# Optimization experiments

Measured on AMD Instinct MI355X. Metric: run time of the kernel, lower is better.

## Reference

```python
import jax, jax.numpy as jnp
import numpy as np

N, E, D, H, L = 20000, 320000, 128, 8, 3
C = D // H  # per-head channels = 16


def setup_inputs() -> dict:
    key = jax.random.key(0)
    ks = jax.random.split(key, 20)
    s = 1.0 / np.sqrt(D)
    inp = {
        "x": jax.random.normal(ks[0], (N, D), dtype=jnp.float32),
        "edge_index": jax.random.randint(ks[1], (2, E), 0, N, dtype=jnp.int64),
        "Wq": jax.random.normal(ks[2], (L, D, D), dtype=jnp.float32) * s,
        "bq": jnp.zeros((L, D), dtype=jnp.float32),
        "Wk": jax.random.normal(ks[3], (L, D, D), dtype=jnp.float32) * s,
        "bk": jnp.zeros((L, D), dtype=jnp.float32),
        "Wv": jax.random.normal(ks[4], (L, D, D), dtype=jnp.float32) * s,
        "bv": jnp.zeros((L, D), dtype=jnp.float32),
        "Wskip": jax.random.normal(ks[5], (L, D, D), dtype=jnp.float32) * s,
        "bskip": jnp.zeros((L, D), dtype=jnp.float32),
        "Wbeta": jax.random.normal(ks[6], (L, 3 * D, 1), dtype=jnp.float32) * (1.0 / np.sqrt(3 * D)),
        "ln_g": jnp.ones((L, D), dtype=jnp.float32),
        "ln_b": jnp.zeros((L, D), dtype=jnp.float32),
        "Wout": jax.random.normal(ks[7], (D, D), dtype=jnp.float32) * s,
        "bout": jnp.zeros((D,), dtype=jnp.float32),
    }
    return inp


def _layer_norm(x, g, b, eps=1e-5):
    mu = jnp.mean(x, axis=-1, keepdims=True)
    var = jnp.mean(jnp.square(x - mu), axis=-1, keepdims=True)
    return (x - mu) * jax.lax.rsqrt(var + eps) * g + b


def _transformer_conv(x, src, dst, Wq, bq, Wk, bk, Wv, bv, Wskip, bskip, Wbeta):
    # project q/k/v: [N, D] -> [N, H, C]
    q = (x @ Wq + bq).reshape(N, H, C)
    k = (x @ Wk + bk).reshape(N, H, C)
    v = (x @ Wv + bv).reshape(N, H, C)
    # per-edge attention logits: [E, H]
    alpha = jnp.sum(q[dst] * k[src], axis=-1) / np.sqrt(C)
    # scatter-softmax over edges grouped by dst node
    m = jax.ops.segment_max(alpha, dst, num_segments=N)  # [N, H]
    m = jnp.where(jnp.isfinite(m), m, 0.0)
    ea = jnp.exp(alpha - m[dst])
    denom = jax.ops.segment_sum(ea, dst, num_segments=N)  # [N, H]
    attn = ea / (denom[dst] + 1e-16)  # [E, H]
    # weighted message aggregation: [N, H, C] -> [N, D]
    out = jax.ops.segment_sum(attn[:, :, None] * v[src], dst, num_segments=N)
    out = out.reshape(N, D)
    # beta-gated skip connection (beta=True, root_weight=True)
    x_r = x @ Wskip + bskip
    beta = jax.nn.sigmoid(jnp.concatenate([out, x_r, out - x_r], axis=-1) @ Wbeta)  # [N, 1]
    return beta * x_r + (1.0 - beta) * out


def reference(x, edge_index, Wq, bq, Wk, bk, Wv, bv, Wskip, bskip, Wbeta, ln_g, ln_b, Wout, bout):
    src, dst = edge_index[0], edge_index[1]
    for i in range(L):
        residual = x
        x = _transformer_conv(x, src, dst, Wq[i], bq[i], Wk[i], bk[i], Wv[i], bv[i],
                              Wskip[i], bskip[i], Wbeta[i])
        x = jax.nn.relu(x)  # dropout is identity in eval mode
        x = _layer_norm(x + residual, ln_g[i], ln_b[i])
    return x @ Wout + bout
```

## Files before the change

kernel.cpp:

```cpp
#include <hip/hip_runtime.h>

#define N_NODES 20000
#define N_EDGES 320000
#define DIM 128
#define NLAYER 3
#define SCAN_BLK 1024
#define N_SCAN_BLKS ((N_NODES + SCAN_BLK - 1) / SCAN_BLK)
#define LDS_STRIDE 136

#define PREP_CASTX_BLKS 2500
#define PREP_CASTW_BLKS 208
#define PREP_ZERO_BLKS 79
#define PREP_TOTAL (PREP_CASTX_BLKS + PREP_CASTW_BLKS + PREP_ZERO_BLKS)

typedef __attribute__((ext_vector_type(8))) short short8;
typedef __attribute__((ext_vector_type(4))) float f32x4;

__device__ inline ushort f2bf(float f) {
  uint u = __float_as_uint(f);
  uint r = (u + 0x7fffu + ((u >> 16) & 1u)) >> 16;
  return (ushort)r;
}
__device__ inline float bf2f(ushort u) { return __uint_as_float(((uint)u) << 16); }

__global__ __launch_bounds__(256) void prep_kernel(
    const float* __restrict__ x, ushort* __restrict__ xb,
    const float* __restrict__ Wq, const float* __restrict__ Wk,
    const float* __restrict__ Wv, const float* __restrict__ Ws,
    const float* __restrict__ Wo, ushort* __restrict__ wt,
    int* __restrict__ degc) {
  int b = blockIdx.x;
  int t = threadIdx.x;
  if (b < PREP_CASTX_BLKS) {
    int i = b * 256 + t;
    float4 f = ((const float4*)x)[i];
    ushort4 o;
    o.x = f2bf(f.x); o.y = f2bf(f.y); o.z = f2bf(f.z); o.w = f2bf(f.w);
    ((ushort4*)xb)[i] = o;
  } else if (b < PREP_CASTX_BLKS + PREP_CASTW_BLKS) {
    int idx = b - PREP_CASTX_BLKS;
    int z = idx >> 4;
    int r = idx & 15;
    int k0 = (r >> 2) * 32, n0 = (r & 3) * 32;
    const float* src;
    if (z < 12) {
      int l = z >> 2, j = z & 3;
      src = (j == 0 ? Wq : j == 1 ? Wk : j == 2 ? Wv : Ws) + (size_t)l * DIM * DIM;
    } else {
      src = Wo;
    }
    __shared__ float tile[32][33];
    int tx = t & 31, ty = t >> 5;
    #pragma unroll
    for (int i = 0; i < 32; i += 8)
      tile[ty + i][tx] = src[(size_t)(k0 + ty + i) * DIM + n0 + tx];
    __syncthreads();
    ushort* dst = wt + (size_t)z * DIM * DIM;
    #pragma unroll
    for (int i = 0; i < 32; i += 8)
      dst[(size_t)(n0 + ty + i) * DIM + k0 + tx] = f2bf(tile[tx][ty + i]);
  } else {
    int i = (b - PREP_CASTX_BLKS - PREP_CASTW_BLKS) * 256 + t;
    if (i < N_NODES) degc[i] = 0;
  }
}


__global__ void count_deg_kernel(const int* __restrict__ ei, int* __restrict__ deg) {
  int e = blockIdx.x * 256 + threadIdx.x;
  if (e < N_EDGES) atomicAdd(&deg[ei[N_EDGES + e]], 1);
}

__global__ __launch_bounds__(SCAN_BLK) void scan1_kernel(const int* __restrict__ deg,
                                                         int* __restrict__ rowptr,
                                                         int* __restrict__ blksum) {
  __shared__ int wsum[16];
  int t = threadIdx.x, lane = t & 63, w = t >> 6;
  int i = blockIdx.x * SCAN_BLK + t;
  int val = (i < N_NODES) ? deg[i] : 0;
  int s = val;
  #pragma unroll
  for (int off = 1; off < 64; off <<= 1) {
    int u = __shfl_up(s, off);
    if (lane >= off) s += u;
  }
  if (lane == 63) wsum[w] = s;
  __syncthreads();
  if (t < 16) {
    int wv = wsum[t];
    int ss = wv;
    #pragma unroll
    for (int off = 1; off < 16; off <<= 1) {
      int u = __shfl_up(ss, off);
      if (t >= off) ss += u;
    }
    wsum[t] = ss - wv;
  }
  __syncthreads();
  int excl = wsum[w] + s - val;
  if (i < N_NODES) rowptr[i] = excl;
  if (t == SCAN_BLK - 1) blksum[blockIdx.x] = excl + val;
}

__global__ void scan2_kernel(int* __restrict__ blksum, int* __restrict__ rowptr) {
  int t = threadIdx.x;
  int val = (t < N_SCAN_BLKS) ? blksum[t] : 0;
  int s = val;
  #pragma unroll
  for (int off = 1; off < 64; off <<= 1) {
    int u = __shfl_up(s, off);
    if (t >= off) s += u;
  }
  if (t < N_SCAN_BLKS) blksum[t] = s - val;
  if (t == 63) rowptr[N_NODES] = s;
}

__global__ __launch_bounds__(SCAN_BLK) void scan3_kernel(int* __restrict__ rowptr,
                                                         const int* __restrict__ blksum,
                                                         int* __restrict__ degc) {
  int i = blockIdx.x * SCAN_BLK + threadIdx.x;
  if (i < N_NODES) {
    rowptr[i] += blksum[blockIdx.x];
    degc[i] = 0;
  }
}

__global__ void scatter_kernel(const int* __restrict__ ei, const int* __restrict__ rowptr,
                               int* __restrict__ cursor, int* __restrict__ csr_src) {
  int e = blockIdx.x * 256 + threadIdx.x;
  if (e < N_EDGES) {
    int d = ei[N_EDGES + e];
    int s = ei[e];
    int pos = atomicAdd(&cursor[d], 1);
    csr_src[rowptr[d] + pos] = s;
  }
}

template <int OUT_BF16>
__global__ __launch_bounds__(256) void gemm_mfma_kernel(
    const ushort* __restrict__ X, const ushort* __restrict__ WT,
    const float* __restrict__ B0, const float* __restrict__ B1,
    const float* __restrict__ B2, const float* __restrict__ B3,
    void* __restrict__ O0, void* __restrict__ O1, void* __restrict__ O2,
    void* __restrict__ O3, int st0, int st1, int st2, int st3) {
  __shared__ ushort As[128 * LDS_STRIDE];
  int mat = blockIdx.y;
  const ushort* Wt = WT + (size_t)mat * DIM * DIM;
  const float* bias;
  void* O;
  int ost;
  switch (mat) {
    case 0: bias = B0; O = O0; ost = st0; break;
    case 1: bias = B1; O = O1; ost = st1; break;
    case 2: bias = B2; O = O2; ost = st2; break;
    default: bias = B3; O = O3; ost = st3; break;
  }
  int t = threadIdx.x;
  int wid = t >> 6, lane = t & 63;
  int row0 = blockIdx.x * 128;
  int wr = wid >> 1, wc = wid & 1;
  int lr = lane & 15;
  int kc8 = (lane >> 4) * 8;

  {
    int rowi = t >> 4;
    int col = (t & 15) * 8;
    #pragma unroll
    for (int pass = 0; pass < 8; ++pass) {
      int row = pass * 16 + rowi;
      int gr = min(row0 + row, N_NODES - 1);
      short8 val = *(const short8*)(X + (size_t)gr * DIM + col);
      *(short8*)(As + row * LDS_STRIDE + col) = val;
    }
  }
  __syncthreads();

  f32x4 acc[4][4];
  #pragma unroll
  for (int i = 0; i < 4; ++i)
    #pragma unroll
    for (int j = 0; j < 4; ++j) acc[i][j] = (f32x4){0.f, 0.f, 0.f, 0.f};

  #pragma unroll
  for (int ks = 0; ks < 4; ++ks) {
    short8 b[4];
    #pragma unroll
    for (int cf = 0; cf < 4; ++cf) {
      int c = wc * 64 + cf * 16 + lr;
      b[cf] = *(const short8*)(Wt + (size_t)c * DIM + ks * 32 + kc8);
    }
    #pragma unroll
    for (int rf = 0; rf < 4; ++rf) {
      int r = wr * 64 + rf * 16 + lr;
      short8 a = *(const short8*)(As + r * LDS_STRIDE + ks * 32 + kc8);
      #pragma unroll
      for (int cf = 0; cf < 4; ++cf)
        acc[rf][cf] = __builtin_amdgcn_mfma_f32_16x16x32_bf16(a, b[cf], acc[rf][cf], 0, 0, 0);
    }
  }

  #pragma unroll
  for (int cf = 0; cf < 4; ++cf) {
    int c = wc * 64 + cf * 16 + lr;
    float bv = bias[c];
    #pragma unroll
    for (int rf = 0; rf < 4; ++rf) {
      #pragma unroll
      for (int reg = 0; reg < 4; ++reg) {
        int r = row0 + wr * 64 + rf * 16 + (lane >> 4) * 4 + reg;
        if (r < N_NODES) {
          float val = acc[rf][cf][reg] + bv;
          if (OUT_BF16)
            ((ushort*)O)[(size_t)r * ost + c] = f2bf(val);
          else
            ((float*)O)[(size_t)r * ost + c] = val;
        }
      }
    }
  }
}

__global__ __launch_bounds__(256) void attn_fused_kernel(
    const ushort* __restrict__ q, const ushort* __restrict__ kv,
    const ushort* __restrict__ xr, const float* __restrict__ xres,
    const int* __restrict__ rowptr, const int* __restrict__ csr_src,
    const float* __restrict__ wbeta, const float* __restrict__ lng,
    const float* __restrict__ lnb, float* __restrict__ xnext,
    ushort* __restrict__ xnextb) {
  __shared__ float lds_s[4][8][20];
  int w = threadIdx.x >> 6;
  int lane = threadIdx.x & 63;
  int n = blockIdx.x * 4 + w;
  int h = lane & 7, e = lane >> 3;

  const ushort* qrow = q + (size_t)n * DIM + h * 16;
  short8 q0 = *(const short8*)qrow;
  short8 q1 = *(const short8*)(qrow + 8);
  float qf[16];
  #pragma unroll
  for (int i = 0; i < 8; ++i) {
    qf[i] = bf2f((ushort)q0[i]);
    qf[8 + i] = bf2f((ushort)q1[i]);
  }

  int s0 = rowptr[n];
  int deg = rowptr[n + 1] - s0;
  float acc[16];
  #pragma unroll
  for (int i = 0; i < 16; ++i) acc[i] = 0.f;
  float dsum = 0.f;

  for (int base = 0; base < deg; base += 8) {
    int idx = base + e;
    bool valid = idx < deg;
    int src = csr_src[s0 + min(idx, deg - 1)];
    const ushort* kr = kv + (size_t)src * 256 + h * 16;
    short8 ka = *(const short8*)kr;
    short8 kb2 = *(const short8*)(kr + 8);
    short8 va = *(const short8*)(kr + 128);
    short8 vb2 = *(const short8*)(kr + 136);
    float p0 = 0.f, p1 = 0.f;
    #pragma unroll
    for (int i = 0; i < 8; ++i) {
      p0 = fmaf(qf[i], bf2f((ushort)ka[i]), p0);
      p1 = fmaf(qf[8 + i], bf2f((ushort)kb2[i]), p1);
    }
    float ea = __expf((p0 + p1) * 0.25f);
    ea = valid ? ea : 0.f;
    dsum += ea;
    #pragma unroll
    for (int i = 0; i < 8; ++i) {
      acc[i] = fmaf(ea, bf2f((ushort)va[i]), acc[i]);
      acc[8 + i] = fmaf(ea, bf2f((ushort)vb2[i]), acc[8 + i]);
    }
  }

  #pragma unroll
  for (int off = 8; off <= 32; off <<= 1) {
    dsum += __shfl_xor(dsum, off);
    #pragma unroll
    for (int i = 0; i < 16; ++i) acc[i] += __shfl_xor(acc[i], off);
  }
  if (lane < 8) {
    #pragma unroll
    for (int i = 0; i < 16; i += 4)
      *(float4*)&lds_s[w][lane][i] = make_float4(acc[i], acc[i + 1], acc[i + 2], acc[i + 3]);
    lds_s[w][lane][16] = dsum;
  }
  __syncthreads();

  int c0 = lane * 2;
  int hh = lane >> 3, cc = (lane & 7) * 2;
  float2 ov = *(float2*)&lds_s[w][hh][cc];
  float den = lds_s[w][hh][16];
  float inv = 1.f / (den + 1e-16f);
  float o0 = ov.x * inv, o1 = ov.y * inv;

  ushort2 xru = *(const ushort2*)(xr + (size_t)n * DIM + c0);
  float xr0 = bf2f(xru.x), xr1 = bf2f(xru.y);
  float wa0 = wbeta[c0] + wbeta[2 * DIM + c0];
  float wa1 = wbeta[c0 + 1] + wbeta[2 * DIM + c0 + 1];
  float wb0 = wbeta[DIM + c0] - wbeta[2 * DIM + c0];
  float wb1 = wbeta[DIM + c0 + 1] - wbeta[2 * DIM + c0 + 1];
  float bs = o0 * wa0 + o1 * wa1 + xr0 * wb0 + xr1 * wb1;
  #pragma unroll
  for (int off = 1; off < 64; off <<= 1) bs += __shfl_xor(bs, off);
  float beta = 1.f / (1.f + __expf(-bs));
  float y0 = fmaxf(beta * xr0 + (1.f - beta) * o0, 0.f);
  float y1 = fmaxf(beta * xr1 + (1.f - beta) * o1, 0.f);
  float2 rv = *(const float2*)(xres + (size_t)n * DIM + c0);
  y0 += rv.x;
  y1 += rv.y;
  float s = y0 + y1;
  #pragma unroll
  for (int off = 1; off < 64; off <<= 1) s += __shfl_xor(s, off);
  float mu = s * (1.f / 128.f);
  float d0 = y0 - mu, d1 = y1 - mu;
  float vs = d0 * d0 + d1 * d1;
  #pragma unroll
  for (int off = 1; off < 64; off <<= 1) vs += __shfl_xor(vs, off);
  float rstd = rsqrtf(vs * (1.f / 128.f) + 1e-5f);
  float2 g = *(const float2*)(lng + c0);
  float2 b = *(const float2*)(lnb + c0);
  float out0 = d0 * rstd * g.x + b.x;
  float out1 = d1 * rstd * g.y + b.y;
  *(float2*)(xnext + (size_t)n * DIM + c0) = make_float2(out0, out1);
  ushort2 ob;
  ob.x = f2bf(out0);
  ob.y = f2bf(out1);
  *(ushort2*)(xnextb + (size_t)n * DIM + c0) = ob;
}


extern "C" void kernel_launch(void* const* d_in, const int* in_sizes, int n_in,
                              void* d_out, int out_size, void* d_ws, size_t ws_size,
                              hipStream_t stream) {
  const float* x_in = (const float*)d_in[0];
  const int* ei = (const int*)d_in[1];
  const float* Wq = (const float*)d_in[2];
  const float* bq = (const float*)d_in[3];
  const float* Wk = (const float*)d_in[4];
  const float* bk = (const float*)d_in[5];
  const float* Wv = (const float*)d_in[6];
  const float* bv = (const float*)d_in[7];
  const float* Wsk = (const float*)d_in[8];
  const float* bsk = (const float*)d_in[9];
  const float* Wb = (const float*)d_in[10];
  const float* lng = (const float*)d_in[11];
  const float* lnb = (const float*)d_in[12];
  const float* Wout = (const float*)d_in[13];
  const float* bout = (const float*)d_in[14];
  float* out = (float*)d_out;

  char* p = (char*)d_ws;
  auto alloc = [&](size_t bytes) {
    char* r = p;
    p += (bytes + 255) & ~(size_t)255;
    return r;
  };
  const size_t NB2 = (size_t)N_NODES * DIM * 2;
  const size_t NB4 = (size_t)N_NODES * DIM * 4;
  ushort* xbb = (ushort*)alloc(NB2);
  ushort* qb = (ushort*)alloc(NB2);
  ushort* kvb = (ushort*)alloc(NB2 * 2);
  ushort* xrb = (ushort*)alloc(NB2);
  float* xf0 = (float*)alloc(NB4);
  float* xf1 = (float*)alloc(NB4);
  ushort* wt = (ushort*)alloc((size_t)13 * DIM * DIM * 2);
  int* rowptr = (int*)alloc((N_NODES + 1) * 4);
  int* degc = (int*)alloc(N_NODES * 4);
  int* blksum = (int*)alloc(64 * 4);
  int* csr_src = (int*)alloc(N_EDGES * 4);

  prep_kernel<<<PREP_TOTAL, 256, 0, stream>>>(x_in, xbb, Wq, Wk, Wv, Wsk, Wout, wt, degc);

  count_deg_kernel<<<(N_EDGES + 255) / 256, 256, 0, stream>>>(ei, degc);
  scan1_kernel<<<N_SCAN_BLKS, SCAN_BLK, 0, stream>>>(degc, rowptr, blksum);
  scan2_kernel<<<1, 64, 0, stream>>>(blksum, rowptr);
  scan3_kernel<<<N_SCAN_BLKS, SCAN_BLK, 0, stream>>>(rowptr, blksum, degc);
  scatter_kernel<<<(N_EDGES + 255) / 256, 256, 0, stream>>>(ei, rowptr, degc, csr_src);

  const int GX = (N_NODES + 127) / 128;
  const float* xres = x_in;
  float* xfbufs[NLAYER] = {xf0, xf1, xf0};
  for (int l = 0; l < NLAYER; ++l) {
    gemm_mfma_kernel<1><<<dim3(GX, 4), 256, 0, stream>>>(
        xbb, wt + (size_t)l * 4 * DIM * DIM,
        bq + (size_t)l * DIM, bk + (size_t)l * DIM, bv + (size_t)l * DIM,
        bsk + (size_t)l * DIM,
        qb, kvb, kvb + 128, xrb, DIM, 256, 256, DIM);
    attn_fused_kernel<<<N_NODES / 4, 256, 0, stream>>>(
        qb, kvb, xrb, xres, rowptr, csr_src,
        Wb + (size_t)l * 3 * DIM, lng + (size_t)l * DIM, lnb + (size_t)l * DIM,
        xfbufs[l], xbb);
    xres = xfbufs[l];
  }
  gemm_mfma_kernel<0><<<dim3(GX, 1), 256, 0, stream>>>(
      xbb, wt + (size_t)12 * DIM * DIM, bout, bout, bout, bout,
      out, out, out, out, DIM, DIM, DIM, DIM);
}
```

Measured before the change: 217.7 us.

## Store K/V head-major and split attention into per-head gather and epilogue kernels

The QKV GEMM now writes K and V into a head-major layout where each node's 16 K and 16 V values for one head sit together in a 64-byte record. Attention is split into a gather kernel with one block per (head, 4 nodes), where 4 lanes share one edge and 16 edges are processed per step, and a separate epilogue kernel for the beta gate, residual and layer norm. The aim is to make the per-head K/V table small and contiguous, so random gathers hit cache better and the grid has more parallelism. In exchange, the attention output makes an extra fp32 round trip through memory, there is one more launch per layer, and the scattered per-element GEMM stores may coalesce less well.

```diff
diff --git a/kernel.cpp b/kernel.cpp
--- a/kernel.cpp
+++ b/kernel.cpp
@@ -142,18 +142,18 @@
     const float* __restrict__ B0, const float* __restrict__ B1,
     const float* __restrict__ B2, const float* __restrict__ B3,
     void* __restrict__ O0, void* __restrict__ O1, void* __restrict__ O2,
-    void* __restrict__ O3, int st0, int st1, int st2, int st3) {
+    void* __restrict__ O3, int m0, int m1, int m2, int m3) {
   __shared__ ushort As[128 * LDS_STRIDE];
   int mat = blockIdx.y;
   const ushort* Wt = WT + (size_t)mat * DIM * DIM;
   const float* bias;
   void* O;
-  int ost;
+  int mode;
   switch (mat) {
-    case 0: bias = B0; O = O0; ost = st0; break;
-    case 1: bias = B1; O = O1; ost = st1; break;
-    case 2: bias = B2; O = O2; ost = st2; break;
-    default: bias = B3; O = O3; ost = st3; break;
+    case 0: bias = B0; O = O0; mode = m0; break;
+    case 1: bias = B1; O = O1; mode = m1; break;
+    case 2: bias = B2; O = O2; mode = m2; break;
+    default: bias = B3; O = O3; mode = m3; break;
   }
   int t = threadIdx.x;
   int wid = t >> 6, lane = t & 63;
@@ -210,91 +210,79 @@
         int r = row0 + wr * 64 + rf * 16 + (lane >> 4) * 4 + reg;
         if (r < N_NODES) {
           float val = acc[rf][cf][reg] + bv;
-          if (OUT_BF16)
-            ((ushort*)O)[(size_t)r * ost + c] = f2bf(val);
-          else
-            ((float*)O)[(size_t)r * ost + c] = val;
+          if (OUT_BF16) {
+            ushort v16 = f2bf(val);
+            if (mode == 0)
+              ((ushort*)O)[(size_t)r * DIM + c] = v16;
+            else
+              ((ushort*)O)[(size_t)(c >> 4) * (N_NODES * 32) + (size_t)r * 32 +
+                           (c & 15) + (mode == 2 ? 16 : 0)] = v16;
+          } else {
+            ((float*)O)[(size_t)r * DIM + c] = val;
+          }
         }
       }
     }
   }
 }
 
-__global__ __launch_bounds__(256) void attn_fused_kernel(
-    const ushort* __restrict__ q, const ushort* __restrict__ kv,
-    const ushort* __restrict__ xr, const float* __restrict__ xres,
+__global__ __launch_bounds__(256) void attn_gather_kernel(
+    const ushort* __restrict__ q, const ushort* __restrict__ kvh,
     const int* __restrict__ rowptr, const int* __restrict__ csr_src,
-    const float* __restrict__ wbeta, const float* __restrict__ lng,
-    const float* __restrict__ lnb, float* __restrict__ xnext,
-    ushort* __restrict__ xnextb) {
-  __shared__ float lds_s[4][8][20];
-  int w = threadIdx.x >> 6;
-  int lane = threadIdx.x & 63;
-  int n = blockIdx.x * 4 + w;
-  int h = lane & 7, e = lane >> 3;
-
-  const ushort* qrow = q + (size_t)n * DIM + h * 16;
-  short8 q0 = *(const short8*)qrow;
-  short8 q1 = *(const short8*)(qrow + 8);
-  float qf[16];
-  #pragma unroll
-  for (int i = 0; i < 8; ++i) {
-    qf[i] = bf2f((ushort)q0[i]);
-    qf[8 + i] = bf2f((ushort)q1[i]);
-  }
-
+    float* __restrict__ aout) {
+  int w = threadIdx.x >> 6, lane = threadIdx.x & 63;
+  int h = blockIdx.x & 7;
+  int n = (blockIdx.x >> 3) * 4 + w;
+  int e = lane >> 2, qq = lane & 3;
+  ushort4 qu = *(const ushort4*)(q + (size_t)n * DIM + h * 16 + qq * 4);
+  float qf0 = bf2f(qu.x), qf1 = bf2f(qu.y), qf2 = bf2f(qu.z), qf3 = bf2f(qu.w);
   int s0 = rowptr[n];
   int deg = rowptr[n + 1] - s0;
-  float acc[16];
-  #pragma unroll
-  for (int i = 0; i < 16; ++i) acc[i] = 0.f;
-  float dsum = 0.f;
-
-  for (int base = 0; base < deg; base += 8) {
-    int idx = base + e;
+  const ushort* bh = kvh + (size_t)h * (N_NODES * 32);
+  float dsum = 0.f, va0 = 0.f, va1 = 0.f, va2 = 0.f, va3 = 0.f;
+  for (int b0 = 0; b0 < deg; b0 += 16) {
+    int idx = b0 + e;
     bool valid = idx < deg;
     int src = csr_src[s0 + min(idx, deg - 1)];
-    const ushort* kr = kv + (size_t)src * 256 + h * 16;
-    short8 ka = *(const short8*)kr;
-    short8 kb2 = *(const short8*)(kr + 8);
-    short8 va = *(const short8*)(kr + 128);
-    short8 vb2 = *(const short8*)(kr + 136);
-    float p0 = 0.f, p1 = 0.f;
-    #pragma unroll
-    for (int i = 0; i < 8; ++i) {
-      p0 = fmaf(qf[i], bf2f((ushort)ka[i]), p0);
-      p1 = fmaf(qf[8 + i], bf2f((ushort)kb2[i]), p1);
-    }
-    float ea = __expf((p0 + p1) * 0.25f);
+    const ushort* rec = bh + (size_t)src * 32 + qq * 4;
+    ushort4 ku = *(const ushort4*)rec;
+    ushort4 vu = *(const ushort4*)(rec + 16);
+    float part = qf0 * bf2f(ku.x) + qf1 * bf2f(ku.y) + qf2 * bf2f(ku.z) + qf3 * bf2f(ku.w);
+    part += __shfl_xor(part, 1);
+    part += __shfl_xor(part, 2);
+    float ea = __expf(part * 0.25f);
     ea = valid ? ea : 0.f;
     dsum += ea;
-    #pragma unroll
-    for (int i = 0; i < 8; ++i) {
-      acc[i] = fmaf(ea, bf2f((ushort)va[i]), acc[i]);
-      acc[8 + i] = fmaf(ea, bf2f((ushort)vb2[i]), acc[8 + i]);
-    }
-  }
-
-  #pragma unroll
-  for (int off = 8; off <= 32; off <<= 1) {
+    va0 = fmaf(ea, bf2f(vu.x), va0);
+    va1 = fmaf(ea, bf2f(vu.y), va1);
+    va2 = fmaf(ea, bf2f(vu.z), va2);
+    va3 = fmaf(ea, bf2f(vu.w), va3);
+  }
+  #pragma unroll
+  for (int off = 4; off <= 32; off <<= 1) {
     dsum += __shfl_xor(dsum, off);
-    #pragma unroll
-    for (int i = 0; i < 16; ++i) acc[i] += __shfl_xor(acc[i], off);
-  }
-  if (lane < 8) {
-    #pragma unroll
-    for (int i = 0; i < 16; i += 4)
-      *(float4*)&lds_s[w][lane][i] = make_float4(acc[i], acc[i + 1], acc[i + 2], acc[i + 3]);
-    lds_s[w][lane][16] = dsum;
-  }
-  __syncthreads();
-
+    va0 += __shfl_xor(va0, off);
+    va1 += __shfl_xor(va1, off);
+    va2 += __shfl_xor(va2, off);
+    va3 += __shfl_xor(va3, off);
+  }
+  if (e == 0) {
+    float inv = 1.f / (dsum + 1e-16f);
+    float4 o = make_float4(va0 * inv, va1 * inv, va2 * inv, va3 * inv);
+    *(float4*)(aout + (size_t)n * DIM + h * 16 + qq * 4) = o;
+  }
+}
+
+__global__ __launch_bounds__(256) void attn_epi_kernel(
+    const float* __restrict__ aout, const ushort* __restrict__ xr,
+    const float* __restrict__ xres, const float* __restrict__ wbeta,
+    const float* __restrict__ lng, const float* __restrict__ lnb,
+    float* __restrict__ xnext, ushort* __restrict__ xnextb) {
+  int w = threadIdx.x >> 6, lane = threadIdx.x & 63;
+  int n = blockIdx.x * 4 + w;
   int c0 = lane * 2;
-  int hh = lane >> 3, cc = (lane & 7) * 2;
-  float2 ov = *(float2*)&lds_s[w][hh][cc];
-  float den = lds_s[w][hh][16];
-  float inv = 1.f / (den + 1e-16f);
-  float o0 = ov.x * inv, o1 = ov.y * inv;
+  float2 ov = *(const float2*)(aout + (size_t)n * DIM + c0);
+  float o0 = ov.x, o1 = ov.y;
 
   ushort2 xru = *(const ushort2*)(xr + (size_t)n * DIM + c0);
   float xr0 = bf2f(xru.x), xr1 = bf2f(xru.y);
@@ -362,8 +350,9 @@
   const size_t NB4 = (size_t)N_NODES * DIM * 4;
   ushort* xbb = (ushort*)alloc(NB2);
   ushort* qb = (ushort*)alloc(NB2);
-  ushort* kvb = (ushort*)alloc(NB2 * 2);
+  ushort* kvh = (ushort*)alloc(NB2 * 2);
   ushort* xrb = (ushort*)alloc(NB2);
+  float* aout = (float*)alloc(NB4);
   float* xf0 = (float*)alloc(NB4);
   float* xf1 = (float*)alloc(NB4);
   ushort* wt = (ushort*)alloc((size_t)13 * DIM * DIM * 2);
@@ -388,14 +377,16 @@
         xbb, wt + (size_t)l * 4 * DIM * DIM,
         bq + (size_t)l * DIM, bk + (size_t)l * DIM, bv + (size_t)l * DIM,
         bsk + (size_t)l * DIM,
-        qb, kvb, kvb + 128, xrb, DIM, 256, 256, DIM);
-    attn_fused_kernel<<<N_NODES / 4, 256, 0, stream>>>(
-        qb, kvb, xrb, xres, rowptr, csr_src,
+        qb, kvh, kvh, xrb, 0, 1, 2, 0);
+    attn_gather_kernel<<<(N_NODES / 4) * 8, 256, 0, stream>>>(
+        qb, kvh, rowptr, csr_src, aout);
+    attn_epi_kernel<<<N_NODES / 4, 256, 0, stream>>>(
+        aout, xrb, xres,
         Wb + (size_t)l * 3 * DIM, lng + (size_t)l * DIM, lnb + (size_t)l * DIM,
         xfbufs[l], xbb);
     xres = xfbufs[l];
   }
   gemm_mfma_kernel<0><<<dim3(GX, 1), 256, 0, stream>>>(
       xbb, wt + (size_t)12 * DIM * DIM, bout, bout, bout, bout,
-      out, out, out, out, DIM, DIM, DIM, DIM);
-}
+      out, out, out, out, 0, 0, 0, 0);
+}
```

Result: slower. 306.6 us (+40.8%).

## Fuse input cast into first GEMM, prefetch CSR indices, replace shuffle reduction with LDS

Applied to the files above, without the earlier changes.

Drops the separate fp32-to-bf16 cast of x from the prep kernel; the first layer's GEMM now reads fp32 x directly and converts while staging it into LDS. The attention kernel folds the 1/sqrt(C) scale into q, prefetches the next edge-chunk's source index one iteration ahead, and replaces the xor-shuffle reduction across edge lanes with per-lane LDS stores followed by an 8-way summation. The intent is to remove an extra pass over x, hide index-load latency, and cut many cross-lane shuffles, at the cost of more LDS traffic. The reduction now relies on an lgkmcnt wait instead of __syncthreads, which is safe only because each wave reads back only its own slice of LDS.

```diff
diff --git a/kernel.cpp b/kernel.cpp
--- a/kernel.cpp
+++ b/kernel.cpp
@@ -8,10 +8,9 @@
 #define N_SCAN_BLKS ((N_NODES + SCAN_BLK - 1) / SCAN_BLK)
 #define LDS_STRIDE 136
 
-#define PREP_CASTX_BLKS 2500
 #define PREP_CASTW_BLKS 208
 #define PREP_ZERO_BLKS 79
-#define PREP_TOTAL (PREP_CASTX_BLKS + PREP_CASTW_BLKS + PREP_ZERO_BLKS)
+#define PREP_TOTAL (PREP_CASTW_BLKS + PREP_ZERO_BLKS)
 
 typedef __attribute__((ext_vector_type(8))) short short8;
 typedef __attribute__((ext_vector_type(4))) float f32x4;
@@ -24,23 +23,15 @@
 __device__ inline float bf2f(ushort u) { return __uint_as_float(((uint)u) << 16); }
 
 __global__ __launch_bounds__(256) void prep_kernel(
-    const float* __restrict__ x, ushort* __restrict__ xb,
     const float* __restrict__ Wq, const float* __restrict__ Wk,
     const float* __restrict__ Wv, const float* __restrict__ Ws,
     const float* __restrict__ Wo, ushort* __restrict__ wt,
     int* __restrict__ degc) {
   int b = blockIdx.x;
   int t = threadIdx.x;
-  if (b < PREP_CASTX_BLKS) {
-    int i = b * 256 + t;
-    float4 f = ((const float4*)x)[i];
-    ushort4 o;
-    o.x = f2bf(f.x); o.y = f2bf(f.y); o.z = f2bf(f.z); o.w = f2bf(f.w);
-    ((ushort4*)xb)[i] = o;
-  } else if (b < PREP_CASTX_BLKS + PREP_CASTW_BLKS) {
-    int idx = b - PREP_CASTX_BLKS;
-    int z = idx >> 4;
-    int r = idx & 15;
+  if (b < PREP_CASTW_BLKS) {
+    int z = b >> 4;
+    int r = b & 15;
     int k0 = (r >> 2) * 32, n0 = (r & 3) * 32;
     const float* src;
     if (z < 12) {
@@ -60,7 +51,7 @@
     for (int i = 0; i < 32; i += 8)
       dst[(size_t)(n0 + ty + i) * DIM + k0 + tx] = f2bf(tile[tx][ty + i]);
   } else {
-    int i = (b - PREP_CASTX_BLKS - PREP_CASTW_BLKS) * 256 + t;
+    int i = (b - PREP_CASTW_BLKS) * 256 + t;
     if (i < N_NODES) degc[i] = 0;
   }
 }
@@ -136,9 +127,9 @@
   }
 }
 
-template <int OUT_BF16>
+template <int OUT_BF16, int IN_F32>
 __global__ __launch_bounds__(256) void gemm_mfma_kernel(
-    const ushort* __restrict__ X, const ushort* __restrict__ WT,
+    const void* __restrict__ Xp, const ushort* __restrict__ WT,
     const float* __restrict__ B0, const float* __restrict__ B1,
     const float* __restrict__ B2, const float* __restrict__ B3,
     void* __restrict__ O0, void* __restrict__ O1, void* __restrict__ O2,
@@ -162,7 +153,21 @@
   int lr = lane & 15;
   int kc8 = (lane >> 4) * 8;
 
-  {
+  if (IN_F32) {
+    const float* Xf = (const float*)Xp;
+    int rowi = t >> 5;
+    int col4 = (t & 31) * 4;
+    #pragma unroll
+    for (int pass = 0; pass < 16; ++pass) {
+      int row = pass * 8 + rowi;
+      int gr = min(row0 + row, N_NODES - 1);
+      float4 f = *(const float4*)(Xf + (size_t)gr * DIM + col4);
+      ushort4 u;
+      u.x = f2bf(f.x); u.y = f2bf(f.y); u.z = f2bf(f.z); u.w = f2bf(f.w);
+      *(ushort4*)(As + row * LDS_STRIDE + col4) = u;
+    }
+  } else {
+    const ushort* X = (const ushort*)Xp;
     int rowi = t >> 4;
     int col = (t & 15) * 8;
     #pragma unroll
@@ -227,7 +232,7 @@
     const float* __restrict__ wbeta, const float* __restrict__ lng,
     const float* __restrict__ lnb, float* __restrict__ xnext,
     ushort* __restrict__ xnextb) {
-  __shared__ float lds_s[4][8][20];
+  __shared__ float red[4][8][8][20];
   int w = threadIdx.x >> 6;
   int lane = threadIdx.x & 63;
   int n = blockIdx.x * 4 + w;
@@ -239,8 +244,8 @@
   float qf[16];
   #pragma unroll
   for (int i = 0; i < 8; ++i) {
-    qf[i] = bf2f((ushort)q0[i]);
-    qf[8 + i] = bf2f((ushort)q1[i]);
+    qf[i] = bf2f((ushort)q0[i]) * 0.25f;
+    qf[8 + i] = bf2f((ushort)q1[i]) * 0.25f;
   }
 
   int s0 = rowptr[n];
@@ -250,10 +255,13 @@
   for (int i = 0; i < 16; ++i) acc[i] = 0.f;
   float dsum = 0.f;
 
+  int src_n = (deg > 0) ? csr_src[s0 + min(e, deg - 1)] : 0;
   for (int base = 0; base < deg; base += 8) {
     int idx = base + e;
     bool valid = idx < deg;
-    int src = csr_src[s0 + min(idx, deg - 1)];
+    int src = src_n;
+    if (base + 8 < deg)
+      src_n = csr_src[s0 + min(base + 8 + e, deg - 1)];
     const ushort* kr = kv + (size_t)src * 256 + h * 16;
     short8 ka = *(const short8*)kr;
     short8 kb2 = *(const short8*)(kr + 8);
@@ -265,7 +273,7 @@
       p0 = fmaf(qf[i], bf2f((ushort)ka[i]), p0);
       p1 = fmaf(qf[8 + i], bf2f((ushort)kb2[i]), p1);
     }
-    float ea = __expf((p0 + p1) * 0.25f);
+    float ea = __expf(p0 + p1);
     ea = valid ? ea : 0.f;
     dsum += ea;
     #pragma unroll
@@ -275,26 +283,29 @@
     }
   }
 
-  #pragma unroll
-  for (int off = 8; off <= 32; off <<= 1) {
-    dsum += __shfl_xor(dsum, off);
-    #pragma unroll
-    for (int i = 0; i < 16; ++i) acc[i] += __shfl_xor(acc[i], off);
-  }
-  if (lane < 8) {
-    #pragma unroll
-    for (int i = 0; i < 16; i += 4)
-      *(float4*)&lds_s[w][lane][i] = make_float4(acc[i], acc[i + 1], acc[i + 2], acc[i + 3]);
-    lds_s[w][lane][16] = dsum;
-  }
-  __syncthreads();
+  {
+    float* my = &red[w][e][h][0];
+    *(float4*)(my + 0) = make_float4(acc[0], acc[1], acc[2], acc[3]);
+    *(float4*)(my + 4) = make_float4(acc[4], acc[5], acc[6], acc[7]);
+    *(float4*)(my + 8) = make_float4(acc[8], acc[9], acc[10], acc[11]);
+    *(float4*)(my + 12) = make_float4(acc[12], acc[13], acc[14], acc[15]);
+    my[16] = dsum;
+  }
+  asm volatile("s_waitcnt lgkmcnt(0)" ::: "memory");
 
   int c0 = lane * 2;
   int hh = lane >> 3, cc = (lane & 7) * 2;
-  float2 ov = *(float2*)&lds_s[w][hh][cc];
-  float den = lds_s[w][hh][16];
+  float o0 = 0.f, o1 = 0.f, den = 0.f;
+  #pragma unroll
+  for (int ee = 0; ee < 8; ++ee) {
+    float2 tv = *(float2*)&red[w][ee][hh][cc];
+    o0 += tv.x;
+    o1 += tv.y;
+    den += red[w][ee][hh][16];
+  }
   float inv = 1.f / (den + 1e-16f);
-  float o0 = ov.x * inv, o1 = ov.y * inv;
+  o0 *= inv;
+  o1 *= inv;
 
   ushort2 xru = *(const ushort2*)(xr + (size_t)n * DIM + c0);
   float xr0 = bf2f(xru.x), xr1 = bf2f(xru.y);
@@ -372,7 +383,7 @@
   int* blksum = (int*)alloc(64 * 4);
   int* csr_src = (int*)alloc(N_EDGES * 4);
 
-  prep_kernel<<<PREP_TOTAL, 256, 0, stream>>>(x_in, xbb, Wq, Wk, Wv, Wsk, Wout, wt, degc);
+  prep_kernel<<<PREP_TOTAL, 256, 0, stream>>>(Wq, Wk, Wv, Wsk, Wout, wt, degc);
 
   count_deg_kernel<<<(N_EDGES + 255) / 256, 256, 0, stream>>>(ei, degc);
   scan1_kernel<<<N_SCAN_BLKS, SCAN_BLK, 0, stream>>>(degc, rowptr, blksum);
@@ -384,18 +395,27 @@
   const float* xres = x_in;
   float* xfbufs[NLAYER] = {xf0, xf1, xf0};
   for (int l = 0; l < NLAYER; ++l) {
-    gemm_mfma_kernel<1><<<dim3(GX, 4), 256, 0, stream>>>(
-        xbb, wt + (size_t)l * 4 * DIM * DIM,
-        bq + (size_t)l * DIM, bk + (size_t)l * DIM, bv + (size_t)l * DIM,
-        bsk + (size_t)l * DIM,
-        qb, kvb, kvb + 128, xrb, DIM, 256, 256, DIM);
+    const void* xin_l = (l == 0) ? (const void*)x_in : (const void*)xbb;
+    if (l == 0) {
+      gemm_mfma_kernel<1, 1><<<dim3(GX, 4), 256, 0, stream>>>(
+          xin_l, wt + (size_t)l * 4 * DIM * DIM,
+          bq + (size_t)l * DIM, bk + (size_t)l * DIM, bv + (size_t)l * DIM,
+          bsk + (size_t)l * DIM,
+          qb, kvb, kvb + 128, xrb, DIM, 256, 256, DIM);
+    } else {
+      gemm_mfma_kernel<1, 0><<<dim3(GX, 4), 256, 0, stream>>>(
+          xin_l, wt + (size_t)l * 4 * DIM * DIM,
+          bq + (size_t)l * DIM, bk + (size_t)l * DIM, bv + (size_t)l * DIM,
+          bsk + (size_t)l * DIM,
+          qb, kvb, kvb + 128, xrb, DIM, 256, 256, DIM);
+    }
     attn_fused_kernel<<<N_NODES / 4, 256, 0, stream>>>(
         qb, kvb, xrb, xres, rowptr, csr_src,
         Wb + (size_t)l * 3 * DIM, lng + (size_t)l * DIM, lnb + (size_t)l * DIM,
         xfbufs[l], xbb);
     xres = xfbufs[l];
   }
-  gemm_mfma_kernel<0><<<dim3(GX, 1), 256, 0, stream>>>(
+  gemm_mfma_kernel<0, 0><<<dim3(GX, 1), 256, 0, stream>>>(
       xbb, wt + (size_t)12 * DIM * DIM, bout, bout, bout, bout,
       out, out, out, out, DIM, DIM, DIM, DIM);
 }
```

New measurement: 207.8 us. 4.6% less time.
